# Performance work log

Hardware: AMD Instinct MI355X
Metric: run time of the kernel (lower is better)

## Reference

```python
import jax, jax.numpy as jnp
import numpy as np


def setup_inputs() -> dict:
    key = jax.random.key(0)
    k1, k2, k3 = jax.random.split(key, 3)
    B, C, H, W = 8, 64, 112, 112
    kh, kw = 5, 5
    return {
        "x": jax.random.normal(k1, (B, C, H, W), dtype=jnp.float32),
        "weight": jax.random.normal(k2, (C, kh, kw), dtype=jnp.float32),
        "bias": jax.random.normal(k3, (C,), dtype=jnp.float32),
        "sign": jnp.ones((1,), dtype=jnp.float32),
        "padding": 2,
        "stride": 1,
        "func_type": 1,
        "alpha": 1,
    }


def _morpho(x, weight, bias, sign, padding, stride, func_type, alpha):
    B, C, H, W = x.shape
    kh, kw = weight.shape[-2:]
    ph = pw = padding
    sh = sw = stride
    H2 = (H + 2 * ph - kh) // sh + 1
    W2 = (W + 2 * pw - kw) // sw + 1
    # sign handling: m*sign*x + (1-m)*x == (m*sign + (1-m)) * x, m detached
    m = jax.lax.stop_gradient((jnp.abs(sign) >= 1e-7).astype(x.dtype))
    s = (m * sign + (1.0 - m)).reshape(-1, 1, 1, 1)  # broadcasts over B or is scalar
    xe = s * x
    xp = jnp.pad(xe, ((0, 0), (0, 0), (ph, ph), (pw, pw)))  # zero pad like F.unfold
    # gather sliding-window taps: [B, C, kh*kw, H2, W2]
    patches = jnp.stack(
        [xp[:, :, i : i + sh * H2 : sh, j : j + sw * W2 : sw]
         for i in range(kh) for j in range(kw)],
        axis=2,
    )
    w = weight.reshape(-1, C, kh * kw, 1, 1)  # (1 or B, C, ks, 1, 1)
    y = patches + w
    if func_type == 0:
        y = y.max(axis=2)
    elif func_type == 1:
        prob = jax.nn.softmax(alpha * y, axis=2)
        y = (y * prob).sum(axis=2)
    elif func_type == 2:
        y = jax.scipy.special.logsumexp(alpha * y, axis=2) / alpha
    else:
        raise NotImplementedError
    if bias is not None:
        y = y + bias.reshape(-1, C, 1, 1)
    y = s * y  # un-apply the sign scaling on the output
    return y  # [B, C, H2, W2]


def reference(x, weight, bias, sign, padding, stride, func_type, alpha):
    return _morpho(x, weight, bias, sign, padding, stride, func_type, alpha)
```

## Files before the change

### kernel.cpp

```cpp
#include <hip/hip_runtime.h>
#include <math.h>

typedef float v2f __attribute__((ext_vector_type(2)));

constexpr int B_  = 8;
constexpr int C_  = 64;
constexpr int H_  = 112;
constexpr int W_  = 112;
constexpr int KH  = 5;
constexpr int KW  = 5;

constexpr int SEG   = 28;
constexpr int NSEG  = 4;
constexpr int NPAIR = 56;
constexpr int STEPS = SEG + KH - 1;
constexpr int TPB   = 256;

__device__ __forceinline__ float uniform_f32(float v) {
    return __int_as_float(__builtin_amdgcn_readfirstlane(__float_as_int(v)));
}

__global__ __launch_bounds__(TPB)
void morpho_stream(const float* __restrict__ x,
                   const float* __restrict__ weight,
                   const float* __restrict__ bias,
                   const float* __restrict__ sign,
                   const int*   __restrict__ alpha_p,
                   float* __restrict__ out)
{
    const int plane = blockIdx.x;
    const int c     = plane & (C_ - 1);
    const int tid   = threadIdx.x;
    if (tid >= NSEG * NPAIR) return;

    const int seg = tid / NPAIR;
    const int g   = tid - seg * NPAIR;
    const int r0  = seg * SEG - 2;
    const int cL  = 2 * g - 2;

    const float sg    = sign[0];
    const float seff  = (fabsf(sg) >= 1e-7f) ? sg : 1.0f;
    const float a     = (float)alpha_p[0];
    const float aK    = a * seff;
    const float inv_a = 1.0f / a;

    const float* xp = x + (size_t)plane * (H_ * W_);
    float*       op = out + (size_t)plane * (H_ * W_);

    const int b0 = (cL < 0) ? 0 : cL;
    const int b1 = cL + 2;
    const int b2 = (cL + 4 > W_ - 2) ? (W_ - 2) : (cL + 4);
    bool cok[6];
#pragma unroll
    for (int j = 0; j < 6; ++j) cok[j] = (cL + j >= 0) && (cL + j < W_);

    v2f xv[3][3];
#pragma unroll
    for (int m = 0; m < 2; ++m) {
        int gr = min(max(r0 + m, 0), H_ - 1);
        const float* row = xp + gr * W_;
        xv[m][0] = *reinterpret_cast<const v2f*>(row + b0);
        xv[m][1] = *reinterpret_cast<const v2f*>(row + b1);
        xv[m][2] = *reinterpret_cast<const v2f*>(row + b2);
    }

    const float* wp = weight + c * (KH * KW);
    float su[KH * KW], sv[KH * KW];
#pragma unroll
    for (int k = 0; k < KH * KW; ++k) {
        float wv = wp[k];
        float u  = __expf(a * wv);
        su[k] = uniform_f32(u);
        sv[k] = uniform_f32(wv * u);
    }
    const float sb = seff * bias[c];

    v2f   acc[5][2];
    float nm2[5][2];
#pragma unroll
    for (int s5 = 0; s5 < 5; ++s5)
#pragma unroll
        for (int c2 = 0; c2 < 2; ++c2) { acc[s5][c2] = (v2f){0.0f, 0.0f}; nm2[s5][c2] = 0.0f; }

#pragma unroll
    for (int i = 0; i < STEPS; ++i) {
        if (i + 2 < STEPS) {
            int gr = min(max(r0 + i + 2, 0), H_ - 1);
            const float* row = xp + gr * W_;
            xv[(i + 2) % 3][0] = *reinterpret_cast<const v2f*>(row + b0);
            xv[(i + 2) % 3][1] = *reinterpret_cast<const v2f*>(row + b1);
            xv[(i + 2) % 3][2] = *reinterpret_cast<const v2f*>(row + b2);
        }

        const int  r   = r0 + i;
        const bool rok = (r >= 0) && (r < H_);
        v2f ew[6];
#pragma unroll
        for (int j = 0; j < 6; ++j) {
            float xj = xv[i % 3][j >> 1][j & 1];
            float ax = (rok && cok[j]) ? aK * xj : 0.0f;
            float e  = __expf(ax);
            ew[j] = (v2f){e, ax * e};
        }

#pragma unroll
        for (int k = 0; k < KH; ++k) {
            const int d = i - k;
            if (d < 0 || d >= SEG) continue;
            const int s5 = d % 5;
#pragma unroll
            for (int j = 0; j < KW; ++j) {
                const float u  = su[k * 5 + j];
                const v2f   u2 = (v2f){u, u};
                const float v  = sv[k * 5 + j];
#pragma unroll
                for (int c2 = 0; c2 < 2; ++c2) {
                    acc[s5][c2] = __builtin_elementwise_fma(u2, ew[c2 + j], acc[s5][c2]);
                    nm2[s5][c2] = fmaf(v, ew[c2 + j].x, nm2[s5][c2]);
                }
            }
        }

        if (i >= 4) {
            const int d  = i - 4;
            const int s5 = d % 5;
            const int ro = seg * SEG + d;
            float v0, v1;
            {
                float Z   = acc[s5][0].x;
                float num = fmaf(acc[s5][0].y, inv_a, nm2[s5][0]);
                v0 = fmaf(seff * num, __builtin_amdgcn_rcpf(Z), sb);
            }
            {
                float Z   = acc[s5][1].x;
                float num = fmaf(acc[s5][1].y, inv_a, nm2[s5][1]);
                v1 = fmaf(seff * num, __builtin_amdgcn_rcpf(Z), sb);
            }
            *reinterpret_cast<v2f*>(op + (size_t)ro * W_ + 2 * g) = (v2f){v0, v1};
            acc[s5][0] = (v2f){0.0f, 0.0f};
            acc[s5][1] = (v2f){0.0f, 0.0f};
            nm2[s5][0] = 0.0f;
            nm2[s5][1] = 0.0f;
        }
    }
}

extern "C" void kernel_launch(void* const* d_in, const int* in_sizes, int n_in,
                              void* d_out, int out_size, void* d_ws, size_t ws_size,
                              hipStream_t stream) {
    const float* x      = (const float*)d_in[0];
    const float* weight = (const float*)d_in[1];
    const float* bias   = (const float*)d_in[2];
    const float* sign   = (const float*)d_in[3];
    const int*   alpha  = (const int*)d_in[7];
    float* out = (float*)d_out;

    dim3 grid(B_ * C_);
    morpho_stream<<<grid, TPB, 0, stream>>>(x, weight, bias, sign, alpha, out);
}
```

Before: 26.93 us.

## Split planes into 8 wave-sized row segments and deepen the row prefetch ring

```diff
diff --git a/kernel.cpp b/kernel.cpp
--- a/kernel.cpp
+++ b/kernel.cpp
@@ -10,33 +10,38 @@
 constexpr int KH  = 5;
 constexpr int KW  = 5;
 
-constexpr int SEG   = 28;
-constexpr int NSEG  = 4;
-constexpr int NPAIR = 56;
-constexpr int STEPS = SEG + KH - 1;
-constexpr int TPB   = 256;
+constexpr int SEG    = 14;
+constexpr int NSEG   = 8;
+constexpr int STEPS  = SEG + KH - 1;
+constexpr int NPAIR  = 56;
+constexpr int TPB    = 256;
+constexpr int NTASK  = B_ * C_ * NSEG;
+constexpr int DEPTH  = 4;
+constexpr int RING   = 5;
 
 __device__ __forceinline__ float uniform_f32(float v) {
     return __int_as_float(__builtin_amdgcn_readfirstlane(__float_as_int(v)));
 }
 
 __global__ __launch_bounds__(TPB)
-void morpho_stream(const float* __restrict__ x,
-                   const float* __restrict__ weight,
-                   const float* __restrict__ bias,
-                   const float* __restrict__ sign,
-                   const int*   __restrict__ alpha_p,
-                   float* __restrict__ out)
+void morpho_stream4(const float* __restrict__ x,
+                    const float* __restrict__ weight,
+                    const float* __restrict__ bias,
+                    const float* __restrict__ sign,
+                    const int*   __restrict__ alpha_p,
+                    float* __restrict__ out)
 {
-    const int plane = blockIdx.x;
+    const int wv    = threadIdx.x >> 6;
+    const int lane  = threadIdx.x & 63;
+    const int task  = blockIdx.x * 4 + wv;
+    const int plane = task >> 3;
+    const int seg   = task & 7;
     const int c     = plane & (C_ - 1);
-    const int tid   = threadIdx.x;
-    if (tid >= NSEG * NPAIR) return;
 
-    const int seg = tid / NPAIR;
-    const int g   = tid - seg * NPAIR;
-    const int r0  = seg * SEG - 2;
-    const int cL  = 2 * g - 2;
+    const bool active = (lane < NPAIR);
+    const int  g   = active ? lane : (NPAIR - 1);
+    const int  r0  = seg * SEG - 2;
+    const int  cL  = 2 * g - 2;
 
     const float sg    = sign[0];
     const float seff  = (fabsf(sg) >= 1e-7f) ? sg : 1.0f;
@@ -54,9 +59,9 @@
 #pragma unroll
     for (int j = 0; j < 6; ++j) cok[j] = (cL + j >= 0) && (cL + j < W_);
 
-    v2f xv[3][3];
+    v2f xv[RING][3];
 #pragma unroll
-    for (int m = 0; m < 2; ++m) {
+    for (int m = 0; m < DEPTH; ++m) {
         int gr = min(max(r0 + m, 0), H_ - 1);
         const float* row = xp + gr * W_;
         xv[m][0] = *reinterpret_cast<const v2f*>(row + b0);
@@ -68,10 +73,10 @@
     float su[KH * KW], sv[KH * KW];
 #pragma unroll
     for (int k = 0; k < KH * KW; ++k) {
-        float wv = wp[k];
-        float u  = __expf(a * wv);
+        float wvv = wp[k];
+        float u   = __expf(a * wvv);
         su[k] = uniform_f32(u);
-        sv[k] = uniform_f32(wv * u);
+        sv[k] = uniform_f32(wvv * u);
     }
     const float sb = seff * bias[c];
 
@@ -84,20 +89,22 @@
 
 #pragma unroll
     for (int i = 0; i < STEPS; ++i) {
-        if (i + 2 < STEPS) {
-            int gr = min(max(r0 + i + 2, 0), H_ - 1);
+        if (i + DEPTH < STEPS) {
+            int gr = min(max(r0 + i + DEPTH, 0), H_ - 1);
             const float* row = xp + gr * W_;
-            xv[(i + 2) % 3][0] = *reinterpret_cast<const v2f*>(row + b0);
-            xv[(i + 2) % 3][1] = *reinterpret_cast<const v2f*>(row + b1);
-            xv[(i + 2) % 3][2] = *reinterpret_cast<const v2f*>(row + b2);
+            const int ws = (i + DEPTH) % RING;
+            xv[ws][0] = *reinterpret_cast<const v2f*>(row + b0);
+            xv[ws][1] = *reinterpret_cast<const v2f*>(row + b1);
+            xv[ws][2] = *reinterpret_cast<const v2f*>(row + b2);
         }
 
         const int  r   = r0 + i;
         const bool rok = (r >= 0) && (r < H_);
+        const int  rs  = i % RING;
         v2f ew[6];
 #pragma unroll
         for (int j = 0; j < 6; ++j) {
-            float xj = xv[i % 3][j >> 1][j & 1];
+            float xj = xv[rs][j >> 1][j & 1];
             float ax = (rok && cok[j]) ? aK * xj : 0.0f;
             float e  = __expf(ax);
             ew[j] = (v2f){e, ax * e};
@@ -125,18 +132,19 @@
             const int d  = i - 4;
             const int s5 = d % 5;
             const int ro = seg * SEG + d;
-            float v0, v1;
+            float o0, o1;
             {
                 float Z   = acc[s5][0].x;
                 float num = fmaf(acc[s5][0].y, inv_a, nm2[s5][0]);
-                v0 = fmaf(seff * num, __builtin_amdgcn_rcpf(Z), sb);
+                o0 = fmaf(seff * num, __builtin_amdgcn_rcpf(Z), sb);
             }
             {
                 float Z   = acc[s5][1].x;
                 float num = fmaf(acc[s5][1].y, inv_a, nm2[s5][1]);
-                v1 = fmaf(seff * num, __builtin_amdgcn_rcpf(Z), sb);
+                o1 = fmaf(seff * num, __builtin_amdgcn_rcpf(Z), sb);
             }
-            *reinterpret_cast<v2f*>(op + (size_t)ro * W_ + 2 * g) = (v2f){v0, v1};
+            if (active)
+                *reinterpret_cast<v2f*>(op + (size_t)ro * W_ + 2 * g) = (v2f){o0, o1};
             acc[s5][0] = (v2f){0.0f, 0.0f};
             acc[s5][1] = (v2f){0.0f, 0.0f};
             nm2[s5][0] = 0.0f;
@@ -155,6 +163,6 @@
     const int*   alpha  = (const int*)d_in[7];
     float* out = (float*)d_out;
 
-    dim3 grid(B_ * C_);
-    morpho_stream<<<grid, TPB, 0, stream>>>(x, weight, bias, sign, alpha, out);
+    dim3 grid(NTASK / 4);
+    morpho_stream4<<<grid, TPB, 0, stream>>>(x, weight, bias, sign, alpha, out);
 }
```

Result: slower. 27.93 us (+3.7%).
